# Performance work log

Hardware: AMD Instinct MI355X
Metric: run time of the kernel (lower is better)

The kernel has to match this reference:

```python
import jax, jax.numpy as jnp
import numpy as np

D_IN = 3
HID = 256
N_BRANCH = 8
SKIP_IN = (4,)
CSG_TREE = [0, 1, [2, 3], [4, 5, [6, 7]]]
FLAG_CONVEX = True
BETA = 100.0
N_POINTS = 100000

# layer dims: [3, 256*7, 8]; layer whose OUTPUT feeds a skip layer emits 256-3=253
_DIMS = [D_IN] + [HID] * 7 + [N_BRANCH]


def _layer_out_dim(layer):
    if (layer + 1) in SKIP_IN:
        return _DIMS[layer + 1] - D_IN
    return _DIMS[layer + 1]


def setup_inputs() -> dict:
    key = jax.random.key(0)
    keys = jax.random.split(key, 20)
    inp = {"x": jax.random.normal(keys[0], (N_POINTS, D_IN), dtype=jnp.float32)}
    n_layers = len(_DIMS) - 1  # 8 linear layers
    for layer in range(n_layers):
        in_d = _DIMS[layer]
        out_d = _layer_out_dim(layer)
        kw = jax.random.fold_in(keys[1], layer)
        if layer == n_layers - 1:  # geometric init of last layer
            W = (np.sqrt(np.pi) / np.sqrt(in_d)
                 + 1e-5 * jax.random.normal(kw, (in_d, out_d), dtype=jnp.float32))
            b = -1.0 * jnp.ones((out_d,), dtype=jnp.float32)
        else:
            W = (np.sqrt(2.0) / np.sqrt(out_d)) * jax.random.normal(
                kw, (in_d, out_d), dtype=jnp.float32)
            b = jnp.zeros((out_d,), dtype=jnp.float32)
        inp[f"W{layer}"] = W
        inp[f"b{layer}"] = b
    return inp


def _softplus_beta(x):
    return jax.nn.softplus(BETA * x) / BETA


def _csg_combine(vals, ops, cvx_flag):
    # hard CSG tree: one-hot matmul == column gather; recursion is static (trace time)
    idxs = [v for v in ops if not isinstance(v, list)]
    cols = [vals[:, jnp.array(idxs)]]
    for v in ops:
        if isinstance(v, list):
            cols.append(_csg_combine(vals, v, not cvx_flag))
    m = jnp.concatenate(cols, axis=1)
    red = jnp.max if cvx_flag else jnp.min
    return red(m, axis=1, keepdims=True)


def _forward(x, Ws, bs):
    inp = x
    h = x
    n_layers = len(Ws)
    inv_sqrt2 = np.float32(1.0 / np.sqrt(2.0))
    for layer in range(n_layers):
        if layer in SKIP_IN:
            h = jnp.concatenate([h, inp], axis=-1) * inv_sqrt2
        h = h @ Ws[layer] + bs[layer]
        if layer < n_layers - 1:
            h = _softplus_beta(h)
    branch_vals = h  # [N, n_branch]
    hcsg = _csg_combine(branch_vals, CSG_TREE, FLAG_CONVEX)  # [N, 1]
    return jnp.concatenate([hcsg, branch_vals], axis=1)  # flag_output == 0


def reference(x, W0, b0, W1, b1, W2, b2, W3, b3, W4, b4, W5, b5, W6, b6, W7, b7):
    Ws = [W0, W1, W2, W3, W4, W5, W6, W7]
    bs = [b0, b1, b2, b3, b4, b5, b6, b7]
    return _forward(x, Ws, bs)
```

## Files before the change

kernel.cpp:

```cpp
#include <hip/hip_runtime.h>
#include <hip/hip_bf16.h>


using bf16x8 = __attribute__((ext_vector_type(8))) __bf16;
using f32x4  = __attribute__((ext_vector_type(4))) float;

#define LDA 264

#define OFFW0 0
#define OFFW1 8192
#define OFFW2 73728
#define OFFW3 139264
#define OFFW4 204800
#define OFFW5 270336
#define OFFW6 335872
#define OFFW7 401408
#define WSB_BYTE_OFF 811008
#define OFFB7 1792

#define SCALE_T2 144.26950408889634f
#define INV_SQRT2 0.70710678118654752f
#define LN2_100 0.0069314718055994531f

__device__ __forceinline__ float fast_exp2(float x) {
#if __has_builtin(__builtin_amdgcn_exp2f)
    return __builtin_amdgcn_exp2f(x);
#else
    return exp2f(x);
#endif
}
__device__ __forceinline__ float fast_log2(float x) {
#if __has_builtin(__builtin_amdgcn_logf)
    return __builtin_amdgcn_logf(x);
#else
    return log2f(x);
#endif
}

__device__ __forceinline__ float softplus_t2(float t2) {
    float e = fast_exp2(-fabsf(t2));
    float l = fast_log2(1.0f + e);
    return fmaxf(t2, 0.0f) + l;
}

__device__ __forceinline__ unsigned short bf16_rne(float f) {
    unsigned int u = __float_as_uint(f);
    unsigned int r = u + 0x7FFFu + ((u >> 16) & 1u);
    return (unsigned short)(r >> 16);
}

template <int KK, int MODE, int NT>
__device__ __forceinline__ void layer_mm(
    const unsigned short* __restrict__ wfrag,
    const float* __restrict__ bias,
    const unsigned short* src, unsigned short* dst,
    const float* xst, int wave, int lane)
{
    const int quad = lane >> 4;
    const int l15  = lane & 15;

    f32x4 acc[2][NT];
#pragma unroll
    for (int i = 0; i < 2; ++i) {
        const int chb = (wave * 2 + i) * 16 + quad * 4;
        const float4 b4 = *(const float4*)(bias + chb);
#pragma unroll
        for (int nt = 0; nt < NT; ++nt)
            acc[i][nt] = f32x4{b4.x, b4.y, b4.z, b4.w};
    }

    const unsigned short* wbase = wfrag + (wave * 2 * KK * 64 + lane) * 8;

#pragma unroll
    for (int kk = 0; kk < KK; ++kk) {
        bf16x8 bfr[NT];
#pragma unroll
        for (int nt = 0; nt < NT; ++nt)
            bfr[nt] = *(const bf16x8*)(src + (nt * 16 + l15) * LDA + kk * 32 + quad * 8);
#pragma unroll
        for (int i = 0; i < 2; ++i) {
            bf16x8 afr = *(const bf16x8*)(wbase + (i * KK + kk) * 512);
#pragma unroll
            for (int nt = 0; nt < NT; ++nt)
                acc[i][nt] = __builtin_amdgcn_mfma_f32_16x16x32_bf16(afr, bfr[nt], acc[i][nt], 0, 0, 0);
        }
    }

#pragma unroll
    for (int i = 0; i < 2; ++i) {
        const int chb = (wave * 2 + i) * 16 + quad * 4;
#pragma unroll
        for (int nt = 0; nt < NT; ++nt) {
            const int pt = nt * 16 + l15;
            float vv[4];
#pragma unroll
            for (int r = 0; r < 4; ++r) {
                float s = softplus_t2(acc[i][nt][r]);
                if (MODE == 1) {
                    const int ch = chb + r;
                    if (ch >= 253)
                        s = xst[pt * 4 + (ch - 253)];
                }
                vv[r] = s;
            }
            __hip_bfloat162 p01 = __float22bfloat162_rn(float2{vv[0], vv[1]});
            __hip_bfloat162 p23 = __float22bfloat162_rn(float2{vv[2], vv[3]});
            uint2 pk;
            pk.x = *(unsigned int*)&p01;
            pk.y = *(unsigned int*)&p23;
            *(uint2*)(dst + pt * LDA + chb) = pk;
        }
    }

    __syncthreads();
}

template <int NT>
__device__ __forceinline__ void run_net(
    const float* __restrict__ x, float* __restrict__ out,
    const unsigned short* __restrict__ wsW, const float* __restrict__ wsB,
    unsigned short* actA, unsigned short* actB, float* xst,
    int base_pt, int npts, int tid)
{
    const int wave = tid >> 6, lane = tid & 63;
    const int quad = lane >> 4, l15 = lane & 15;

    for (int i = tid; i < NT * 16 * 32; i += 512) {
        const int pt = i >> 5, ch = i & 31;
        const int ptg = base_pt + pt;
        float v = 0.0f;
        if (ch < 3 && ptg < npts) v = x[ptg * 3 + ch];
        actA[pt * LDA + ch] = bf16_rne(v);
        if (ch < 4) xst[pt * 4 + ch] = (ch < 3) ? v : 0.0f;
    }
    __syncthreads();

    layer_mm<1, 0, NT>(wsW + OFFW0, wsB + 0 * 256, actA, actB, xst, wave, lane);
    layer_mm<8, 0, NT>(wsW + OFFW1, wsB + 1 * 256, actB, actA, xst, wave, lane);
    layer_mm<8, 0, NT>(wsW + OFFW2, wsB + 2 * 256, actA, actB, xst, wave, lane);
    layer_mm<8, 1, NT>(wsW + OFFW3, wsB + 3 * 256, actB, actA, xst, wave, lane);
    layer_mm<8, 0, NT>(wsW + OFFW4, wsB + 4 * 256, actA, actB, xst, wave, lane);
    layer_mm<8, 0, NT>(wsW + OFFW5, wsB + 5 * 256, actB, actA, xst, wave, lane);
    layer_mm<8, 0, NT>(wsW + OFFW6, wsB + 6 * 256, actA, actB, xst, wave, lane);

    if (wave < NT) {
        const float4 b4 = *(const float4*)(wsB + OFFB7 + quad * 4);
        f32x4 acc = f32x4{b4.x, b4.y, b4.z, b4.w};
        const unsigned short* w7 = wsW + OFFW7;
#pragma unroll
        for (int kk = 0; kk < 8; ++kk) {
            bf16x8 bfr = *(const bf16x8*)(actB + (wave * 16 + l15) * LDA + kk * 32 + quad * 8);
            bf16x8 afr = *(const bf16x8*)(w7 + (kk * 64 + lane) * 8);
            acc = __builtin_amdgcn_mfma_f32_16x16x32_bf16(afr, bfr, acc, 0, 0, 0);
        }
        float u0 = __shfl(acc[0], l15 + 16);
        float u1 = __shfl(acc[1], l15 + 16);
        float u2 = __shfl(acc[2], l15 + 16);
        float u3 = __shfl(acc[3], l15 + 16);
        if (quad == 0) {
            const int ptg = base_pt + wave * 16 + l15;
            if (ptg < npts) {
                const float v0 = acc[0], v1 = acc[1], v2 = acc[2], v3 = acc[3];
                const float v4 = u0, v5 = u1, v6 = u2, v7 = u3;
                const float m23   = fminf(v2, v3);
                const float m67   = fmaxf(v6, v7);
                const float m4567 = fminf(fminf(v4, v5), m67);
                const float h     = fmaxf(fmaxf(v0, v1), fmaxf(m23, m4567));
                float* o = out + (long)ptg * 9;
                o[0] = h;
                o[1] = v0; o[2] = v1; o[3] = v2; o[4] = v3;
                o[5] = v4; o[6] = v5; o[7] = v6; o[8] = v7;
            }
        }
    }
}

__global__ __launch_bounds__(512, 4)
void nhrep_main(const float* __restrict__ x, float* __restrict__ out,
                const unsigned short* __restrict__ wsW,
                const float* __restrict__ wsB, int npts, int nbig)
{
    __shared__ unsigned short actA[64 * LDA];
    __shared__ unsigned short actB[64 * LDA];
    __shared__ float xst[64 * 4];
    const int b = blockIdx.x;
    if (b < nbig) {
        run_net<4>(x, out, wsW, wsB, actA, actB, xst, b * 64, npts, threadIdx.x);
    } else {
        run_net<2>(x, out, wsW, wsB, actA, actB, xst,
                   nbig * 64 + (b - nbig) * 32, npts, threadIdx.x);
    }
}

struct PackArgs {
    const float* W[8];
    const float* b[8];
};

#define TOTAL_FRAGS 50688
#define TOTAL_BIAS  1808

__global__ void prepack_all(PackArgs args, unsigned short* __restrict__ dstW,
                            float* __restrict__ dstB)
{
    const int t = blockIdx.x * blockDim.x + threadIdx.x;
    const int FB[9]  = {0, 1024, 9216, 17408, 25600, 33792, 41984, 50176, 50688};
    const int KKs[8] = {1, 8, 8, 8, 8, 8, 8, 8};
    const int ind[8] = {3, 256, 256, 256, 256, 256, 256, 256};
    const int outd[8]= {256, 256, 256, 253, 256, 256, 256, 8};

    if (t < TOTAL_FRAGS) {
        int l = 0;
        while (t >= FB[l + 1]) ++l;
        const int f    = t - FB[l];
        const int lane = f & 63;
        const int kk   = (f >> 6) % KKs[l];
        const int mt   = f / (64 * KKs[l]);
        const int o    = mt * 16 + (lane & 15);
        const int kb   = kk * 32 + (lane >> 4) * 8;
        const float* W = args.W[l];
        const int in_d = ind[l], out_d = outd[l];

        unsigned short v[8];
#pragma unroll
        for (int j = 0; j < 8; ++j) {
            const int k = kb + j;
            float w = 0.0f;
            if (k < in_d && o < out_d) {
                float sc = 1.0f;
                if (l == 0) sc = SCALE_T2;
                else if (l == 4) sc = (k < 253) ? INV_SQRT2 : (SCALE_T2 * INV_SQRT2);
                else if (l == 7) sc = LN2_100;
                w = W[k * out_d + o] * sc;
            }
            unsigned int u = __float_as_uint(w);
            v[j] = (unsigned short)((u + 0x7FFFu + ((u >> 16) & 1u)) >> 16);
        }
        uint4 p;
        p.x = (unsigned int)v[0] | ((unsigned int)v[1] << 16);
        p.y = (unsigned int)v[2] | ((unsigned int)v[3] << 16);
        p.z = (unsigned int)v[4] | ((unsigned int)v[5] << 16);
        p.w = (unsigned int)v[6] | ((unsigned int)v[7] << 16);
        *(uint4*)(dstW + (long)t * 8) = p;
    } else if (t < TOTAL_FRAGS + TOTAL_BIAS) {
        const int u = t - TOTAL_FRAGS;
        const int l = (u < 1792) ? (u >> 8) : 7;
        const int idx = (l < 7) ? (u & 255) : (u - 1792);
        const float sc = (l < 7) ? SCALE_T2 : 1.0f;
        dstB[u] = (idx < outd[l]) ? args.b[l][idx] * sc : 0.0f;
    }
}

extern "C" void kernel_launch(void* const* d_in, const int* in_sizes, int n_in,
                              void* d_out, int out_size, void* d_ws, size_t ws_size,
                              hipStream_t stream)
{
    const float* x = (const float*)d_in[0];
    unsigned short* wsW = (unsigned short*)d_ws;
    float* wsB = (float*)((char*)d_ws + WSB_BYTE_OFF);

    PackArgs pa;
    for (int l = 0; l < 8; ++l) {
        pa.W[l] = (const float*)d_in[1 + 2 * l];
        pa.b[l] = (const float*)d_in[2 + 2 * l];
    }
    const int ptot = TOTAL_FRAGS + TOTAL_BIAS;
    prepack_all<<<(ptot + 255) / 256, 256, 0, stream>>>(pa, wsW, wsB);

    const int npts = in_sizes[0] / 3;
    int nbig, nsmall;
    const int tail_pts = 16384;
    if (npts > tail_pts) {
        nbig = (npts - tail_pts + 63) / 64;
        const int base_small = nbig * 64;
        nsmall = (npts - base_small + 31) / 32;
    } else {
        nbig = 0;
        nsmall = (npts + 31) / 32;
    }
    nhrep_main<<<nbig + nsmall, 512, 0, stream>>>(x, (float*)d_out, wsW, wsB,
                                                  npts, nbig);
}
```

Measured before the change: 193.9 us.

## Use single in-place activation buffer and enlarge big tiles to 96 points

The ping-pong activation buffers are replaced by one shared buffer updated in place, with an extra barrier between the MFMA reads and the softplus writes. The freed LDS is used to grow big blocks from 64 to 96 points (NT=6), so each weight fragment loaded from global/L2 is reused across more points. The cost is an extra __syncthreads per layer, more accumulator registers per thread (which may hurt occupancy under the 4-block launch bound), and fewer, larger blocks.

```diff
diff --git a/kernel.cpp b/kernel.cpp
--- a/kernel.cpp
+++ b/kernel.cpp
@@ -9,11 +9,6 @@
 
 #define OFFW0 0
 #define OFFW1 8192
-#define OFFW2 73728
-#define OFFW3 139264
-#define OFFW4 204800
-#define OFFW5 270336
-#define OFFW6 335872
 #define OFFW7 401408
 #define WSB_BYTE_OFF 811008
 #define OFFB7 1792
@@ -53,8 +48,8 @@
 __device__ __forceinline__ void layer_mm(
     const unsigned short* __restrict__ wfrag,
     const float* __restrict__ bias,
-    const unsigned short* src, unsigned short* dst,
-    const float* xst, int wave, int lane)
+    unsigned short* act, const float* xst,
+    int wave, int lane)
 {
     const int quad = lane >> 4;
     const int l15  = lane & 15;
@@ -76,7 +71,7 @@
         bf16x8 bfr[NT];
 #pragma unroll
         for (int nt = 0; nt < NT; ++nt)
-            bfr[nt] = *(const bf16x8*)(src + (nt * 16 + l15) * LDA + kk * 32 + quad * 8);
+            bfr[nt] = *(const bf16x8*)(act + (nt * 16 + l15) * LDA + kk * 32 + quad * 8);
 #pragma unroll
         for (int i = 0; i < 2; ++i) {
             bf16x8 afr = *(const bf16x8*)(wbase + (i * KK + kk) * 512);
@@ -85,6 +80,8 @@
                 acc[i][nt] = __builtin_amdgcn_mfma_f32_16x16x32_bf16(afr, bfr[nt], acc[i][nt], 0, 0, 0);
         }
     }
+
+    __syncthreads();
 
 #pragma unroll
     for (int i = 0; i < 2; ++i) {
@@ -108,7 +105,7 @@
             uint2 pk;
             pk.x = *(unsigned int*)&p01;
             pk.y = *(unsigned int*)&p23;
-            *(uint2*)(dst + pt * LDA + chb) = pk;
+            *(uint2*)(act + pt * LDA + chb) = pk;
         }
     }
 
@@ -119,7 +116,7 @@
 __device__ __forceinline__ void run_net(
     const float* __restrict__ x, float* __restrict__ out,
     const unsigned short* __restrict__ wsW, const float* __restrict__ wsB,
-    unsigned short* actA, unsigned short* actB, float* xst,
+    unsigned short* act, float* xst,
     int base_pt, int npts, int tid)
 {
     const int wave = tid >> 6, lane = tid & 63;
@@ -130,18 +127,18 @@
         const int ptg = base_pt + pt;
         float v = 0.0f;
         if (ch < 3 && ptg < npts) v = x[ptg * 3 + ch];
-        actA[pt * LDA + ch] = bf16_rne(v);
+        act[pt * LDA + ch] = bf16_rne(v);
         if (ch < 4) xst[pt * 4 + ch] = (ch < 3) ? v : 0.0f;
     }
     __syncthreads();
 
-    layer_mm<1, 0, NT>(wsW + OFFW0, wsB + 0 * 256, actA, actB, xst, wave, lane);
-    layer_mm<8, 0, NT>(wsW + OFFW1, wsB + 1 * 256, actB, actA, xst, wave, lane);
-    layer_mm<8, 0, NT>(wsW + OFFW2, wsB + 2 * 256, actA, actB, xst, wave, lane);
-    layer_mm<8, 1, NT>(wsW + OFFW3, wsB + 3 * 256, actB, actA, xst, wave, lane);
-    layer_mm<8, 0, NT>(wsW + OFFW4, wsB + 4 * 256, actA, actB, xst, wave, lane);
-    layer_mm<8, 0, NT>(wsW + OFFW5, wsB + 5 * 256, actB, actA, xst, wave, lane);
-    layer_mm<8, 0, NT>(wsW + OFFW6, wsB + 6 * 256, actA, actB, xst, wave, lane);
+    layer_mm<1, 0, NT>(wsW + OFFW0, wsB + 0 * 256, act, xst, wave, lane);
+    layer_mm<8, 0, NT>(wsW + OFFW1 + 0 * 65536, wsB + 1 * 256, act, xst, wave, lane);
+    layer_mm<8, 0, NT>(wsW + OFFW1 + 1 * 65536, wsB + 2 * 256, act, xst, wave, lane);
+    layer_mm<8, 1, NT>(wsW + OFFW1 + 2 * 65536, wsB + 3 * 256, act, xst, wave, lane);
+    layer_mm<8, 0, NT>(wsW + OFFW1 + 3 * 65536, wsB + 4 * 256, act, xst, wave, lane);
+    layer_mm<8, 0, NT>(wsW + OFFW1 + 4 * 65536, wsB + 5 * 256, act, xst, wave, lane);
+    layer_mm<8, 0, NT>(wsW + OFFW1 + 5 * 65536, wsB + 6 * 256, act, xst, wave, lane);
 
     if (wave < NT) {
         const float4 b4 = *(const float4*)(wsB + OFFB7 + quad * 4);
@@ -149,7 +146,7 @@
         const unsigned short* w7 = wsW + OFFW7;
 #pragma unroll
         for (int kk = 0; kk < 8; ++kk) {
-            bf16x8 bfr = *(const bf16x8*)(actB + (wave * 16 + l15) * LDA + kk * 32 + quad * 8);
+            bf16x8 bfr = *(const bf16x8*)(act + (wave * 16 + l15) * LDA + kk * 32 + quad * 8);
             bf16x8 afr = *(const bf16x8*)(w7 + (kk * 64 + lane) * 8);
             acc = __builtin_amdgcn_mfma_f32_16x16x32_bf16(afr, bfr, acc, 0, 0, 0);
         }
@@ -180,15 +177,14 @@
                 const unsigned short* __restrict__ wsW,
                 const float* __restrict__ wsB, int npts, int nbig)
 {
-    __shared__ unsigned short actA[64 * LDA];
-    __shared__ unsigned short actB[64 * LDA];
-    __shared__ float xst[64 * 4];
+    __shared__ unsigned short act[96 * LDA];
+    __shared__ float xst[96 * 4];
     const int b = blockIdx.x;
     if (b < nbig) {
-        run_net<4>(x, out, wsW, wsB, actA, actB, xst, b * 64, npts, threadIdx.x);
+        run_net<6>(x, out, wsW, wsB, act, xst, b * 96, npts, threadIdx.x);
     } else {
-        run_net<2>(x, out, wsW, wsB, actA, actB, xst,
-                   nbig * 64 + (b - nbig) * 32, npts, threadIdx.x);
+        run_net<2>(x, out, wsW, wsB, act, xst,
+                   nbig * 96 + (b - nbig) * 32, npts, threadIdx.x);
     }
 }
 
@@ -271,8 +267,8 @@
     int nbig, nsmall;
     const int tail_pts = 16384;
     if (npts > tail_pts) {
-        nbig = (npts - tail_pts + 63) / 64;
-        const int base_small = nbig * 64;
+        nbig = (npts - tail_pts + 95) / 96;
+        const int base_small = nbig * 96;
         nsmall = (npts - base_small + 31) / 32;
     } else {
         nbig = 0;
```

New measurement: 189.1 us. 1.03x faster.
